# Kernel tuning notes

Hardware: AMD Instinct MI355X
Metric: run time of the kernel (lower is better)

The kernel has to match this reference:

```python
import jax, jax.numpy as jnp
import numpy as np

HID = 4096; H = 32; KVH = 8; D = 128
B = 4; Q = 256; KV = 2048; HIST = KV - Q
BS = 64; NB = KV // BS; NBLOCKS = 160
WINDOW = 1024; THETA = 10000.0


def _rope(x, pos):
    # x: [T, heads, D], pos: [T] absolute positions
    half = D // 2
    inv = 1.0 / (THETA ** (jnp.arange(half, dtype=jnp.float32) / half))
    f = pos.astype(jnp.float32)[:, None] * inv[None, :]          # [T, D/2]
    cos = jnp.concatenate([jnp.cos(f), jnp.cos(f)], -1)[:, None, :]
    sin = jnp.concatenate([jnp.sin(f), jnp.sin(f)], -1)[:, None, :]
    x1, x2 = jnp.split(x, 2, axis=-1)
    return x * cos + jnp.concatenate([-x2, x1], -1) * sin


def setup_inputs() -> dict:
    key = jax.random.key(0)
    ks = jax.random.split(key, 7)
    T = B * Q
    return dict(
        hidden_states=jax.random.normal(ks[0], (T, HID), jnp.float32),
        wq=jax.random.normal(ks[1], (HID, H * D), jnp.float32) * 0.02,
        wk=jax.random.normal(ks[2], (HID, KVH * D), jnp.float32) * 0.02,
        wv=jax.random.normal(ks[3], (HID, KVH * D), jnp.float32) * 0.02,
        wo=jax.random.normal(ks[4], (H * D, HID), jnp.float32) * 0.02,
        k_cache=jax.random.normal(ks[5], (NBLOCKS, BS, KVH, D), jnp.float32),
        v_cache=jax.random.normal(ks[6], (NBLOCKS, BS, KVH, D), jnp.float32),
        # each sequence appends Q new tokens at positions [HIST, KV)
        position_ids=jnp.tile(HIST + jnp.arange(Q, dtype=jnp.int32), B),
        q_start_loc=jnp.arange(B, dtype=jnp.int32) * Q,
        q_seq_length=jnp.full((B,), Q, jnp.int32),
        kv_seq_length=jnp.full((B,), KV, jnp.int32),
        block_offsets=jnp.arange(B * NB, dtype=jnp.int32).reshape(B, NB),
    )


def reference(hidden_states, wq, wk, wv, wo, k_cache, v_cache,
              position_ids, q_start_loc, q_seq_length, kv_seq_length,
              block_offsets):
    # qkv proj (no bias, Mistral)
    q = (hidden_states @ wq).reshape(-1, H, D)    # [T, H, D]
    k = (hidden_states @ wk).reshape(-1, KVH, D)  # [T, KVH, D]
    v = (hidden_states @ wv).reshape(-1, KVH, D)
    # rotary embedding on q, k with per-token absolute positions
    q = _rope(q, position_ids)
    k = _rope(k, position_ids)
    # fill paged KV cache: token with in-sequence slot s of sequence b goes to
    # block block_offsets[b, s // BS], offset s % BS
    b_idx = jnp.repeat(jnp.arange(B), Q)
    blk = block_offsets[b_idx, position_ids // BS]
    off = position_ids % BS
    k_cache = k_cache.at[blk, off].set(k)
    v_cache = v_cache.at[blk, off].set(v)
    # paged attention: gather each sequence's blocks from the cache
    k_all = k_cache[block_offsets].reshape(B, KV, KVH, D)
    v_all = v_cache[block_offsets].reshape(B, KV, KVH, D)
    G = H // KVH  # GQA group size
    qb = q.reshape(B, Q, KVH, G, D)
    scores = jnp.einsum('bqhgd,bkhd->bhgqk', qb, k_all) / jnp.sqrt(jnp.float32(D))
    # causal + sliding-window mask on absolute positions
    qpos = HIST + jnp.arange(Q)
    kpos = jnp.arange(KV)
    valid = (kpos[None, :] <= qpos[:, None]) & (kpos[None, :] > qpos[:, None] - WINDOW)
    scores = jnp.where(valid[None, None, None], scores, -jnp.inf)
    p = jax.nn.softmax(scores, axis=-1)
    o = jnp.einsum('bhgqk,bkhd->bqhgd', p, v_all).reshape(B * Q, H * D)
    return o @ wo
```

## Files before the change

kernel.cpp:

```cpp
#include <hip/hip_runtime.h>

#define BSZ  4
#define QL   256
#define KVL  2048
#define HIST 1792
#define WIN  1024
#define NH   32
#define NKVH 8
#define DH   128
#define HID  4096
#define SCALE 0.088388347648318447f
#define MFIX  8.0f

typedef __bf16 bf16x8 __attribute__((ext_vector_type(8)));
typedef float  fx4    __attribute__((ext_vector_type(4)));
typedef unsigned short us4 __attribute__((ext_vector_type(4)));
typedef unsigned short us8 __attribute__((ext_vector_type(8)));

__device__ __forceinline__ unsigned short f2bf(float x) {
    unsigned u = __float_as_uint(x);
    u += 0x7FFFu + ((u >> 16) & 1u);
    return (unsigned short)(u >> 16);
}
__device__ __forceinline__ float bf2f(unsigned short h) {
    return __uint_as_float(((unsigned)h) << 16);
}
__device__ __forceinline__ fx4 mfma16(bf16x8 a, bf16x8 b, fx4 c) {
    return __builtin_amdgcn_mfma_f32_16x16x32_bf16(a, b, c, 0, 0, 0);
}
__device__ __forceinline__ bf16x8 ldb16(const unsigned short* p) {
    return *reinterpret_cast<const bf16x8*>(p);
}

typedef __attribute__((address_space(1))) const void gv_t;
typedef __attribute__((address_space(3))) void lv_t;
__device__ __forceinline__ void gl16(const void* g, void* l) {
    __builtin_amdgcn_global_load_lds((gv_t*)g, (lv_t*)l, 16, 0, 0);
}

__global__ __launch_bounds__(256) void gemm_bf16_kernel(
    const unsigned short* __restrict__ A, const unsigned short* __restrict__ B,
    float* __restrict__ C0, float* __restrict__ Cz, size_t czstride,
    int lda, int ldb, int ldc, int ksteps, int nx, int ny)
{
    constexpr int TILE = 128 * 32;
    __shared__ __align__(16) unsigned short lds[3 * 2 * TILE];

    const int per = gridDim.x >> 3;
    const int t = (blockIdx.x & 7) * per + (blockIdx.x >> 3);
    const int bx = t % nx;
    const int by = (t / nx) % ny;
    const int bz = t / (nx * ny);

    const int row0 = bx * 128;
    const int col0 = by * 128;
    const int kbase = bz * ksteps * 32;
    float* Cm = (bz == 0) ? C0 : (Cz + (size_t)(bz - 1) * czstride);

    const int tid  = threadIdx.x;
    const int lane = tid & 63;
    const int w    = tid >> 6;
    const int wr   = w >> 1, wc = w & 1;
    const int l16  = lane & 15;
    const int lg   = lane >> 4;
    const int r_in = lane >> 2;
    const int c8   = (lane & 3) * 8;

    fx4 acc[4][4] = {};

    auto STAGE = [&](int bufi, int kp) {
        unsigned short* Lb = lds + bufi * (2 * TILE);
#pragma unroll
        for (int i = 0; i < 2; ++i) {
            const int r = w * 32 + i * 16 + r_in;
            const int ldsb = (w * 2 + i) * 512;
            gl16(A + (size_t)(row0 + r) * lda + kp + c8, Lb + ldsb);
            gl16(B + (size_t)(col0 + r) * ldb + kp + c8, Lb + TILE + ldsb);
        }
    };

    STAGE(0, kbase);
    STAGE(1, kbase + 32);
    for (int ks = 0; ks < ksteps; ++ks) {
        if (ks + 2 < ksteps) {
            STAGE((ks + 2) % 3, kbase + (ks + 2) * 32);
            asm volatile("s_waitcnt vmcnt(8)" ::: "memory");
        } else if (ks + 1 < ksteps) {
            asm volatile("s_waitcnt vmcnt(4)" ::: "memory");
        } else {
            asm volatile("s_waitcnt vmcnt(0)" ::: "memory");
        }
        __builtin_amdgcn_s_barrier();
        __builtin_amdgcn_sched_barrier(0);

        const unsigned short* Lb = lds + (ks % 3) * (2 * TILE);
        const unsigned short* AhT = Lb;
        const unsigned short* BhT = Lb + TILE;

        bf16x8 af[4], bfv[4];
#pragma unroll
        for (int f = 0; f < 4; ++f) {
            af[f]  = ldb16(AhT + (wr * 64 + f * 16 + l16) * 32 + lg * 8);
            bfv[f] = ldb16(BhT + (wc * 64 + f * 16 + l16) * 32 + lg * 8);
        }
        __builtin_amdgcn_s_setprio(1);
#pragma unroll
        for (int fr = 0; fr < 4; ++fr)
#pragma unroll
            for (int fc = 0; fc < 4; ++fc)
                acc[fr][fc] = mfma16(af[fr], bfv[fc], acc[fr][fc]);
        __builtin_amdgcn_s_setprio(0);
        __builtin_amdgcn_sched_barrier(0);
        __builtin_amdgcn_s_barrier();
    }
#pragma unroll
    for (int fr = 0; fr < 4; ++fr)
#pragma unroll
        for (int fc = 0; fc < 4; ++fc) {
            const size_t rbase = (size_t)(row0 + wr * 64 + fr * 16 + lg * 4);
            const int col = col0 + wc * 64 + fc * 16 + l16;
#pragma unroll
            for (int r = 0; r < 4; ++r)
                Cm[(rbase + r) * ldc + col] = acc[fr][fc][r];
        }
}

__global__ __launch_bounds__(256) void transpose_w_kernel(
    const float* __restrict__ w, unsigned short* __restrict__ hi, int N)
{
    __shared__ unsigned short sh[64][72];
    const int n0 = blockIdx.x * 64;
    const int k0 = blockIdx.y * 64;
    const int tid = threadIdx.x;
    const int rr = tid >> 4;
    const int cc = (tid & 15) * 4;
#pragma unroll
    for (int p = 0; p < 4; ++p) {
        const int kl = p * 16 + rr;
        fx4 v = *reinterpret_cast<const fx4*>(w + (size_t)(k0 + kl) * N + n0 + cc);
#pragma unroll
        for (int j = 0; j < 4; ++j)
            sh[cc + j][kl] = f2bf(v[j]);
    }
    __syncthreads();
    const int nl = tid >> 2;
    const int kc = (tid & 3) * 16;
    unsigned short* oh = hi + (size_t)(n0 + nl) * 4096 + k0 + kc;
    *reinterpret_cast<us8*>(oh)     = *reinterpret_cast<const us8*>(&sh[nl][kc]);
    *reinterpret_cast<us8*>(oh + 8) = *reinterpret_cast<const us8*>(&sh[nl][kc + 8]);
}

__global__ __launch_bounds__(256) void convert_bf16_kernel(
    const float* __restrict__ in, unsigned short* __restrict__ out, int n4)
{
    int i = blockIdx.x * blockDim.x + threadIdx.x;
    for (; i < n4; i += gridDim.x * blockDim.x) {
        fx4 v = reinterpret_cast<const fx4*>(in)[i];
        us4 o;
#pragma unroll
        for (int j = 0; j < 4; ++j) o[j] = f2bf(v[j]);
        reinterpret_cast<us4*>(out)[i] = o;
    }
}

__global__ void sincos_table_kernel(float* __restrict__ tab)
{
    const int qi = blockIdx.x;
    const int jr = threadIdx.x;
    const float inv = powf(10000.f, -(float)jr * (1.f / 64.f));
    const float f = (float)(HIST + qi) * inv;
    float s, c;
    sincosf(f, &s, &c);
    tab[(qi * 64 + jr) * 2]     = c;
    tab[(qi * 64 + jr) * 2 + 1] = s;
}

__global__ __launch_bounds__(256) void rope_q_kernel(
    const float* __restrict__ qkv0, const float* __restrict__ qkv1,
    const int* __restrict__ pos_ids, const float* __restrict__ tab,
    unsigned short* __restrict__ qb)
{
    const int t = blockIdx.x;
    const int b = t >> 8;
    const int qi = t & 255;
    const int pi = pos_ids[t] - HIST;
    const int tid = threadIdx.x;
    const int h = tid >> 3;
    const int d0 = (tid & 7) * 8;
    const float* q0 = qkv0 + (size_t)t * 6144 + h * DH;
    const float* q1 = qkv1 + (size_t)t * 6144 + h * DH;
    float xl[8], xh[8];
    *reinterpret_cast<fx4*>(&xl[0]) = *reinterpret_cast<const fx4*>(q0 + d0)
                                    + *reinterpret_cast<const fx4*>(q1 + d0);
    *reinterpret_cast<fx4*>(&xl[4]) = *reinterpret_cast<const fx4*>(q0 + d0 + 4)
                                    + *reinterpret_cast<const fx4*>(q1 + d0 + 4);
    *reinterpret_cast<fx4*>(&xh[0]) = *reinterpret_cast<const fx4*>(q0 + d0 + 64)
                                    + *reinterpret_cast<const fx4*>(q1 + d0 + 64);
    *reinterpret_cast<fx4*>(&xh[4]) = *reinterpret_cast<const fx4*>(q0 + d0 + 68)
                                    + *reinterpret_cast<const fx4*>(q1 + d0 + 68);
    us8 outl, outh;
#pragma unroll
    for (int i = 0; i < 8; ++i) {
        const int jr = d0 + i;
        const float c = tab[(pi * 64 + jr) * 2];
        const float s = tab[(pi * 64 + jr) * 2 + 1];
        outl[i] = f2bf(xl[i] * c - xh[i] * s);
        outh[i] = f2bf(xh[i] * c + xl[i] * s);
    }
    unsigned short* dst = qb + (((size_t)b * NH + h) * QL + qi) * DH;
    *reinterpret_cast<us8*>(dst + d0)      = outl;
    *reinterpret_cast<us8*>(dst + d0 + 64) = outh;
}

__global__ __launch_bounds__(256) void gather_kv_kernel(
    const float* __restrict__ qkv0, const float* __restrict__ qkv1,
    const float* __restrict__ k_cache, const float* __restrict__ v_cache,
    const int* __restrict__ block_offsets, const float* __restrict__ tab,
    unsigned short* __restrict__ k_all, unsigned short* __restrict__ vT)
{
    __shared__ unsigned short vls[32][136];
    const int bid = blockIdx.x;
    const int ck = bid & 63;
    const int kh = (bid >> 6) & 7;
    const int b  = bid >> 9;
    const int kv0 = ck * 32;
    const int tid = threadIdx.x;
    const int tok = tid >> 3;
    const int sl  = tid & 7;
    const int kvpos = kv0 + tok;
    const bool is_old = (kvpos < HIST);

    float x[16];
    float v[16];
    if (is_old) {
        const int blk = block_offsets[b * 32 + (kvpos >> 6)];
        const size_t base = (((size_t)blk * 64 + (kvpos & 63)) * NKVH + kh) * DH + sl * 4;
        const float* sk = k_cache + base;
        const float* sv = v_cache + base;
#pragma unroll
        for (int j = 0; j < 4; ++j) {
            *reinterpret_cast<fx4*>(&x[j * 4]) = *reinterpret_cast<const fx4*>(sk + j * 32);
            *reinterpret_cast<fx4*>(&v[j * 4]) = *reinterpret_cast<const fx4*>(sv + j * 32);
        }
    } else {
        const int t = b * QL + (kvpos - HIST);
        const int pi = kvpos - HIST;
        const size_t tb = (size_t)t * 6144 + kh * DH + sl * 4;
        const float* k0p = qkv0 + tb + 4096;
        const float* k1p = qkv1 + tb + 4096;
        const float* v0p = qkv0 + tb + 5120;
        const float* v1p = qkv1 + tb + 5120;
#pragma unroll
        for (int j = 0; j < 4; ++j) {
            *reinterpret_cast<fx4*>(&x[j * 4]) =
                *reinterpret_cast<const fx4*>(k0p + j * 32) +
                *reinterpret_cast<const fx4*>(k1p + j * 32);
            *reinterpret_cast<fx4*>(&v[j * 4]) =
                *reinterpret_cast<const fx4*>(v0p + j * 32) +
                *reinterpret_cast<const fx4*>(v1p + j * 32);
        }
#pragma unroll
        for (int j = 0; j < 2; ++j) {
            const int jr0 = sl * 4 + j * 32;
            fx4 cs0 = *reinterpret_cast<const fx4*>(tab + ((size_t)pi * 64 + jr0) * 2);
            fx4 cs1 = *reinterpret_cast<const fx4*>(tab + ((size_t)pi * 64 + jr0) * 2 + 4);
            const float c[4] = {cs0[0], cs0[2], cs1[0], cs1[2]};
            const float s[4] = {cs0[1], cs0[3], cs1[1], cs1[3]};
#pragma unroll
            for (int e = 0; e < 4; ++e) {
                const float lo = x[j * 4 + e], hi = x[(j + 2) * 4 + e];
                x[j * 4 + e]       = lo * c[e] - hi * s[e];
                x[(j + 2) * 4 + e] = hi * c[e] + lo * s[e];
            }
        }
    }
    {
        const size_t tbase = (((size_t)b * NKVH + kh) * KVL + kv0) * DH;
#pragma unroll
        for (int j = 0; j < 4; ++j) {
            const int d = sl * 4 + j * 32;
            const int dc = d >> 3;
            us4 pk;
#pragma unroll
            for (int e = 0; e < 4; ++e) pk[e] = f2bf(x[j * 4 + e]);
            *reinterpret_cast<us4*>(k_all + tbase + ((dc * 32 + tok) << 3) + (d & 7)) = pk;
        }
    }
#pragma unroll
    for (int j = 0; j < 4; ++j) {
        us4 pv;
#pragma unroll
        for (int e = 0; e < 4; ++e) pv[e] = f2bf(v[j * 4 + e]);
        *reinterpret_cast<us4*>(&vls[tok][sl * 4 + j * 32]) = pv;
    }
    __syncthreads();
    const int dr = tid >> 1;
    const int half = tid & 1;
    const size_t vb = (((size_t)b * NKVH + kh) * DH + dr) * KVL + kv0 + half * 16;
#pragma unroll
    for (int i = 0; i < 16; i += 8) {
        us8 pk;
#pragma unroll
        for (int j = 0; j < 8; ++j) pk[j] = vls[half * 16 + i + j][dr];
        *reinterpret_cast<us8*>(vT + vb + i) = pk;
    }
}

__global__ __launch_bounds__(256) void attn_kernel(
    const unsigned short* __restrict__ qb,
    const unsigned short* __restrict__ kall,
    const unsigned short* __restrict__ vT,
    unsigned short* __restrict__ ohi)
{
    __shared__ __align__(16) unsigned short ldskv[3 * 8192];
    __shared__ __align__(16) unsigned short plds[4][16][40];

    const int bid = blockIdx.x;
    const int xcd = bid & 7, slot = bid >> 3;
    const int pair = xcd * 4 + (slot >> 4);
    const int within = slot & 15;
    const int kh = pair >> 2, b = pair & 3;
    const int qt = within & 3, h = kh * 4 + (within >> 2);

    const int tid = threadIdx.x;
    const int lane = tid & 63;
    const int w = tid >> 6;
    const int l16 = lane & 15;
    const int lg = lane >> 4;
    const int qrow0 = qt * 64 + w * 16;
    const int qabs0 = HIST + qrow0;

    const unsigned short* qptr =
        qb + (((size_t)b * NH + h) * QL + qrow0 + l16) * DH + lg * 8;
    bf16x8 qf[4];
#pragma unroll
    for (int ds = 0; ds < 4; ++ds) qf[ds] = ldb16(qptr + ds * 32);

    fx4 oacc[8];
#pragma unroll
    for (int f = 0; f < 8; ++f) oacc[f] = (fx4){0.f, 0.f, 0.f, 0.f};
    float lsum[4] = {0.f, 0.f, 0.f, 0.f};

    const unsigned short* kbase = kall + ((size_t)b * NKVH + kh) * (KVL * DH);
    const unsigned short* vbase = vT + ((size_t)b * NKVH + kh) * (DH * KVL);

    const int kv_lo = ((HIST + qt * 64) - (WIN - 1)) & ~31;

    auto STAGE = [&](int bufi, int kv0) {
        unsigned short* kl = ldskv + bufi * 8192;
        const unsigned short* kg = kbase + (size_t)kv0 * DH;
#pragma unroll
        for (int j = 0; j < 2; ++j) {
            const int ci = w * 64 + lane + j * 256;
            gl16(kg + ci * 8, kl + w * 512 + j * 2048);
            gl16(vbase + (size_t)(ci >> 2) * KVL + kv0 + (ci & 3) * 8,
                 kl + 4096 + w * 512 + j * 2048);
        }
    };

    STAGE(0, kv_lo);
    STAGE(1, kv_lo + 32);

    for (int t = 0; t < 34; ++t) {
        if (t + 2 < 34) {
            STAGE((t + 2) % 3, kv_lo + (t + 2) * 32);
            asm volatile("s_waitcnt vmcnt(8)" ::: "memory");
        } else if (t + 1 < 34) {
            asm volatile("s_waitcnt vmcnt(4)" ::: "memory");
        } else {
            asm volatile("s_waitcnt vmcnt(0)" ::: "memory");
        }
        __builtin_amdgcn_s_barrier();
        __builtin_amdgcn_sched_barrier(0);

        const unsigned short* kl = ldskv + (t % 3) * 8192;
        const unsigned short* vl = kl + 4096;
        const int kv0 = kv_lo + t * 32;

        fx4 s0 = (fx4){0.f, 0.f, 0.f, 0.f};
        fx4 s1 = (fx4){0.f, 0.f, 0.f, 0.f};
#pragma unroll
        for (int ds = 0; ds < 4; ++ds) {
            bf16x8 kf0 = ldb16(kl + ((ds * 4 + lg) * 32 + l16) * 8);
            bf16x8 kf1 = ldb16(kl + ((ds * 4 + lg) * 32 + 16 + l16) * 8);
            s0 = mfma16(qf[ds], kf0, s0);
            s1 = mfma16(qf[ds], kf1, s1);
        }
        float p0v[4], p1v[4];
        const bool interior = (kv0 >= qabs0 + 16 - WIN) && (kv0 + 31 <= qabs0);
        if (interior) {
#pragma unroll
            for (int r = 0; r < 4; ++r) {
                p0v[r] = __expf(fmaf(s0[r], SCALE, -MFIX));
                p1v[r] = __expf(fmaf(s1[r], SCALE, -MFIX));
            }
        } else {
            const int kvp0 = kv0 + l16, kvp1 = kvp0 + 16;
#pragma unroll
            for (int r = 0; r < 4; ++r) {
                const int qpos = qabs0 + lg * 4 + r;
                const float e0 = __expf(fmaf(s0[r], SCALE, -MFIX));
                const float e1 = __expf(fmaf(s1[r], SCALE, -MFIX));
                p0v[r] = (kvp0 <= qpos && kvp0 > qpos - WIN) ? e0 : 0.f;
                p1v[r] = (kvp1 <= qpos && kvp1 > qpos - WIN) ? e1 : 0.f;
            }
        }
#pragma unroll
        for (int r = 0; r < 4; ++r) {
            lsum[r] += p0v[r] + p1v[r];
            plds[w][lg * 4 + r][l16] = f2bf(p0v[r]);
            plds[w][lg * 4 + r][16 + l16] = f2bf(p1v[r]);
        }
        asm volatile("s_waitcnt lgkmcnt(0)" ::: "memory");
        __builtin_amdgcn_sched_barrier(0);
        bf16x8 pa = ldb16(&plds[w][l16][lg * 8]);
#pragma unroll
        for (int f = 0; f < 8; ++f) {
            bf16x8 vf = ldb16(vl + ((f * 16 + l16) * 4 + lg) * 8);
            oacc[f] = mfma16(pa, vf, oacc[f]);
        }
        __builtin_amdgcn_sched_barrier(0);
        __builtin_amdgcn_s_barrier();
    }
#pragma unroll
    for (int r = 0; r < 4; ++r) {
#pragma unroll
        for (int off = 1; off < 16; off <<= 1)
            lsum[r] += __shfl_xor(lsum[r], off);
    }
    float rl[4];
#pragma unroll
    for (int r = 0; r < 4; ++r) rl[r] = 1.f / lsum[r];
    const size_t obase = ((size_t)b * QL + qrow0 + lg * 4) * (NH * DH) + h * DH;
#pragma unroll
    for (int f = 0; f < 8; ++f)
#pragma unroll
        for (int r = 0; r < 4; ++r)
            ohi[obase + (size_t)r * (NH * DH) + f * 16 + l16] = f2bf(oacc[f][r] * rl[r]);
}

__global__ __launch_bounds__(256) void reduce_out_kernel(
    float* __restrict__ out, const float* __restrict__ parts)
{
    const int n4 = (1024 * 4096) / 4;
    int i = blockIdx.x * blockDim.x + threadIdx.x;
    for (; i < n4; i += gridDim.x * blockDim.x) {
        fx4 v = reinterpret_cast<fx4*>(out)[i] + reinterpret_cast<const fx4*>(parts)[i];
        reinterpret_cast<fx4*>(out)[i] = v;
    }
}

extern "C" void kernel_launch(void* const* d_in, const int* in_sizes, int n_in,
                              void* d_out, int out_size, void* d_ws, size_t ws_size,
                              hipStream_t stream)
{
    const float* hs = (const float*)d_in[0];
    const float* wq = (const float*)d_in[1];
    const float* wk = (const float*)d_in[2];
    const float* wv = (const float*)d_in[3];
    const float* wo = (const float*)d_in[4];
    const float* kc = (const float*)d_in[5];
    const float* vc = (const float*)d_in[6];
    const int* pos  = (const int*)d_in[7];
    const int* boff = (const int*)d_in[11];
    float* out = (float*)d_out;

    char* ws = (char*)d_ws;
    unsigned short* woTh  = (unsigned short*)(ws + 0);
    unsigned short* wqkvT = (unsigned short*)(ws + 67108864);
    unsigned short* kall  = (unsigned short*)(ws + 67108864);
    unsigned short* vTp   = (unsigned short*)(ws + 83886080);
    unsigned short* ohi   = (unsigned short*)(ws + 100663296);
    float* qkvb           = (float*)(ws + 117440512);
    float* oparts         = (float*)(ws + 117440512);
    unsigned short* hsb   = (unsigned short*)(ws + 167772160);
    unsigned short* qbb   = (unsigned short*)(ws + 167772160);
    float* tab            = (float*)(ws + 176160768);

    transpose_w_kernel<<<dim3(64, 64), 256, 0, stream>>>(wq, wqkvT, 4096);
    transpose_w_kernel<<<dim3(16, 64), 256, 0, stream>>>(wk, wqkvT + (size_t)4096 * 4096, 1024);
    transpose_w_kernel<<<dim3(16, 64), 256, 0, stream>>>(wv, wqkvT + (size_t)5120 * 4096, 1024);
    transpose_w_kernel<<<dim3(64, 64), 256, 0, stream>>>(wo, woTh, 4096);
    convert_bf16_kernel<<<2048, 256, 0, stream>>>(hs, hsb, 1048576);
    sincos_table_kernel<<<256, 64, 0, stream>>>(tab);

    gemm_bf16_kernel<<<768, 256, 0, stream>>>(
        hsb, wqkvT,
        qkvb, qkvb + (size_t)1024 * 6144, (size_t)1024 * 6144,
        4096, 4096, 6144, 64, 8, 48);

    rope_q_kernel<<<1024, 256, 0, stream>>>(qkvb, qkvb + 6291456, pos, tab, qbb);
    gather_kv_kernel<<<2048, 256, 0, stream>>>(qkvb, qkvb + 6291456, kc, vc, boff, tab, kall, vTp);
    attn_kernel<<<512, 256, 0, stream>>>(qbb, kall, vTp, ohi);

    gemm_bf16_kernel<<<512, 256, 0, stream>>>(
        ohi, woTh,
        out, oparts, (size_t)1024 * 4096,
        4096, 4096, 4096, 64, 8, 32);
    reduce_out_kernel<<<2048, 256, 0, stream>>>(out, oparts);
}
```

Measured before the change: 250.6 us.

## Tile V transpose into contiguous chunks and split output GEMM three ways along K

The transposed V buffer is now stored as contiguous 32-token tiles of 4096 elements, so the attention kernel's per-step V load becomes one contiguous block instead of 128 strided rows. The output projection GEMM is split into three K-slices (43/43/42 steps) across 768 workgroups instead of two, and the reduction kernel adds the extra partial buffer. The split raises occupancy for the output GEMM but costs an extra partial-sum write and read in the reduction.

```diff
diff --git a/kernel.cpp b/kernel.cpp
--- a/kernel.cpp
+++ b/kernel.cpp
@@ -41,7 +41,7 @@
 __global__ __launch_bounds__(256) void gemm_bf16_kernel(
     const unsigned short* __restrict__ A, const unsigned short* __restrict__ B,
     float* __restrict__ C0, float* __restrict__ Cz, size_t czstride,
-    int lda, int ldb, int ldc, int ksteps, int nx, int ny)
+    int lda, int ldb, int ldc, int ksteps, int klast, int nx, int ny, int nz)
 {
     constexpr int TILE = 128 * 32;
     __shared__ __align__(16) unsigned short lds[3 * 2 * TILE];
@@ -55,6 +55,7 @@
     const int row0 = bx * 128;
     const int col0 = by * 128;
     const int kbase = bz * ksteps * 32;
+    const int nks = (bz == nz - 1) ? klast : ksteps;
     float* Cm = (bz == 0) ? C0 : (Cz + (size_t)(bz - 1) * czstride);
 
     const int tid  = threadIdx.x;
@@ -81,11 +82,11 @@
 
     STAGE(0, kbase);
     STAGE(1, kbase + 32);
-    for (int ks = 0; ks < ksteps; ++ks) {
-        if (ks + 2 < ksteps) {
+    for (int ks = 0; ks < nks; ++ks) {
+        if (ks + 2 < nks) {
             STAGE((ks + 2) % 3, kbase + (ks + 2) * 32);
             asm volatile("s_waitcnt vmcnt(8)" ::: "memory");
-        } else if (ks + 1 < ksteps) {
+        } else if (ks + 1 < nks) {
             asm volatile("s_waitcnt vmcnt(4)" ::: "memory");
         } else {
             asm volatile("s_waitcnt vmcnt(0)" ::: "memory");
@@ -296,13 +297,14 @@
     __syncthreads();
     const int dr = tid >> 1;
     const int half = tid & 1;
-    const size_t vb = (((size_t)b * NKVH + kh) * DH + dr) * KVL + kv0 + half * 16;
+    unsigned short* vtile = vT + (((size_t)b * NKVH + kh) * 64 + ck) * 4096;
 #pragma unroll
     for (int i = 0; i < 16; i += 8) {
+        const int kvc = half * 2 + (i >> 3);
         us8 pk;
 #pragma unroll
         for (int j = 0; j < 8; ++j) pk[j] = vls[half * 16 + i + j][dr];
-        *reinterpret_cast<us8*>(vT + vb + i) = pk;
+        *reinterpret_cast<us8*>(vtile + kvc * 1024 + dr * 8) = pk;
     }
 }
 
@@ -342,19 +344,19 @@
     float lsum[4] = {0.f, 0.f, 0.f, 0.f};
 
     const unsigned short* kbase = kall + ((size_t)b * NKVH + kh) * (KVL * DH);
-    const unsigned short* vbase = vT + ((size_t)b * NKVH + kh) * (DH * KVL);
+    const unsigned short* vbase = vT + ((size_t)b * NKVH + kh) * (KVL * DH);
 
     const int kv_lo = ((HIST + qt * 64) - (WIN - 1)) & ~31;
 
     auto STAGE = [&](int bufi, int kv0) {
         unsigned short* kl = ldskv + bufi * 8192;
         const unsigned short* kg = kbase + (size_t)kv0 * DH;
+        const unsigned short* vg = vbase + (size_t)(kv0 >> 5) * 4096;
 #pragma unroll
         for (int j = 0; j < 2; ++j) {
             const int ci = w * 64 + lane + j * 256;
             gl16(kg + ci * 8, kl + w * 512 + j * 2048);
-            gl16(vbase + (size_t)(ci >> 2) * KVL + kv0 + (ci & 3) * 8,
-                 kl + 4096 + w * 512 + j * 2048);
+            gl16(vg + ci * 8, kl + 4096 + w * 512 + j * 2048);
         }
     };
 
@@ -416,7 +418,7 @@
         bf16x8 pa = ldb16(&plds[w][l16][lg * 8]);
 #pragma unroll
         for (int f = 0; f < 8; ++f) {
-            bf16x8 vf = ldb16(vl + ((f * 16 + l16) * 4 + lg) * 8);
+            bf16x8 vf = ldb16(vl + lg * 1024 + (f * 16 + l16) * 8);
             oacc[f] = mfma16(pa, vf, oacc[f]);
         }
         __builtin_amdgcn_sched_barrier(0);
@@ -445,7 +447,9 @@
     const int n4 = (1024 * 4096) / 4;
     int i = blockIdx.x * blockDim.x + threadIdx.x;
     for (; i < n4; i += gridDim.x * blockDim.x) {
-        fx4 v = reinterpret_cast<fx4*>(out)[i] + reinterpret_cast<const fx4*>(parts)[i];
+        fx4 v = reinterpret_cast<fx4*>(out)[i]
+              + reinterpret_cast<const fx4*>(parts)[i]
+              + reinterpret_cast<const fx4*>(parts)[i + n4];
         reinterpret_cast<fx4*>(out)[i] = v;
     }
 }
@@ -487,15 +491,15 @@
     gemm_bf16_kernel<<<768, 256, 0, stream>>>(
         hsb, wqkvT,
         qkvb, qkvb + (size_t)1024 * 6144, (size_t)1024 * 6144,
-        4096, 4096, 6144, 64, 8, 48);
+        4096, 4096, 6144, 64, 64, 8, 48, 2);
 
     rope_q_kernel<<<1024, 256, 0, stream>>>(qkvb, qkvb + 6291456, pos, tab, qbb);
     gather_kv_kernel<<<2048, 256, 0, stream>>>(qkvb, qkvb + 6291456, kc, vc, boff, tab, kall, vTp);
     attn_kernel<<<512, 256, 0, stream>>>(qbb, kall, vTp, ohi);
 
-    gemm_bf16_kernel<<<512, 256, 0, stream>>>(
+    gemm_bf16_kernel<<<768, 256, 0, stream>>>(
         ohi, woTh,
         out, oparts, (size_t)1024 * 4096,
-        4096, 4096, 4096, 64, 8, 32);
+        4096, 4096, 4096, 43, 42, 8, 32, 3);
     reduce_out_kernel<<<2048, 256, 0, stream>>>(out, oparts);
 }
```

Result: no change. 250.9 us (+0.1%).
